# Kernel optimization log

Hardware: AMD Instinct MI355X
Metric: run time of the kernel (lower is better)

## Reference

```python
import jax, jax.numpy as jnp
import numpy as np
from jax import lax

T = 36          # sequence length
N_POLES = 80    # N -> dictionary has 2N+1 = 161 atoms
LAM = 0.1       # lam_f
MAX_ITER = 100
TOL = 1e-05


def real_D(T, rho, theta):
    # CONSTR=True: squash rho into [0.001, 1.15], theta into [0, pi]
    rmin, rmax = 0.001, 1.15
    r = rmin + (rmax - rmin) * jax.nn.sigmoid(rho)          # (N,)
    th = jnp.pi * jax.nn.sigmoid(theta)                     # (N,)
    i = jnp.arange(T, dtype=rho.dtype)[:, None]             # (T,1)
    p = r[None, :] ** i                                     # (T,N)
    W1 = p * jnp.cos(i * th[None, :])
    W2 = p * jnp.sin(i * th[None, :])
    D = jnp.concatenate([jnp.ones((T, 1), rho.dtype), W1, W2], axis=1)  # (T, 2N+1)
    # NORM=True: column-normalize all but the constant column
    norms = jnp.linalg.norm(D[:, 1:], axis=0, keepdims=True)
    return jnp.concatenate([D[:, :1], D[:, 1:] / norms], axis=1)


def softshrink(v, thr):
    return jnp.sign(v) * jnp.maximum(jnp.abs(v) - thr, 0.0)


def fista_efc(D, Y, lam, max_iter):
    # argmin_C ||Y - D C||_2^2 + lam |C|_1
    DtD = D.T @ D                                           # (P,P)
    L_inv = 1.0 / jnp.linalg.norm(DtD, ord=2)               # 1/spectral norm
    P = DtD.shape[0]
    dim_data = Y.shape[-1]
    A = jnp.eye(P, dtype=Y.dtype) - L_inv * DtD             # (P,P)
    B = L_inv * jnp.einsum('tp,btd->bpd', D, Y)             # (B,P,d)
    thr = lax.stop_gradient(lam * L_inv)                    # .item() in torch => constant

    batch = Y.shape[0]
    x0 = jnp.zeros((batch, P, dim_data), Y.dtype)
    y0 = jnp.zeros((batch, P, dim_data), Y.dtype)

    def body(carry, _):
        x, y, t, done = carry
        x_new = softshrink(jnp.einsum('pq,bqd->bpd', A, y) + B, thr)
        diff = jnp.linalg.norm(x - x_new) / dim_data        # Frobenius over all elems
        t_new = (1.0 + jnp.sqrt(1.0 + 4.0 * t * t)) / 2.0
        tt = (t - 1.0) / t_new
        y_new = (1.0 + tt) * x_new - tt * x
        # if already converged before this step, freeze the state (early return)
        x_out = jnp.where(done, x, x_new)
        y_out = jnp.where(done, y, y_new)
        t_out = jnp.where(done, t, t_new)
        done_new = done | (diff < TOL)
        return (x_out, y_out, t_out, done_new), None

    init = (x0, y0, jnp.float32(1.0), jnp.bool_(False))
    (x_fin, _, _, _), _ = lax.scan(body, init, None, length=max_iter)
    return x_fin


def reference(x, rho, theta):
    # DAN.forward with wiRH=False, freezeD=False
    dic = real_D(T, rho, theta)                             # (T, 2N+1)
    C = fista_efc(dic, x, LAM, MAX_ITER)                    # (B, 2N+1, d)
    reconst = jnp.einsum('tp,bpd->btd', dic, C)             # (B, T, d)
    return C, dic, reconst


def setup_inputs() -> dict:
    key = jax.random.key(0)
    k1, k2, k3 = jax.random.split(key, 3)
    x = jax.random.normal(k1, (256, T, 50), dtype=jnp.float32)
    rho = jax.random.uniform(k2, (N_POLES,), dtype=jnp.float32)
    theta = jax.random.uniform(k3, (N_POLES,), dtype=jnp.float32)
    return {"x": x, "rho": rho, "theta": theta}
```

## Files before the change

### kernel.cpp

```cpp
#include <hip/hip_runtime.h>
#include <math.h>

typedef _Float16 half_t;
typedef __attribute__((ext_vector_type(8))) _Float16 half8;
typedef __attribute__((ext_vector_type(4))) _Float16 half4;
typedef __attribute__((ext_vector_type(4))) float floatx4;

#define TDIM 36
#define PDIM 161
#define NCOL 50
#define NITER 100
#define PITER8 50

#define NKA 5
#define GSTR 44
#define SPS 196

#define YROW 384
#define RROW 128

#define SWZ(row, byteoff) ((byteoff) ^ (((row) & 7) << 4))

#define BY_Y    0
#define BY_R    24576
#define BY_LRTH 28672
#define BY_Y0   32768
#define BY_SC   33024
#define BY_GS   33040
#define BY_G2   39376
#define BY_G4   45712
#define LDS_TOTAL 52048

#define MFMA16 __builtin_amdgcn_mfma_f32_16x16x32_f16

__global__ __launch_bounds__(768, 3)
void dan_kernel(const float* __restrict__ xin, const float* __restrict__ rho,
                const float* __restrict__ theta, float* __restrict__ outC,
                float* __restrict__ outDic, float* __restrict__ outR)
{
  extern __shared__ char smc[];
  float*  sc   = (float*)(smc + BY_SC);
  float*  Gs   = (float*)(smc + BY_GS);
  float*  G2   = (float*)(smc + BY_G2);
  float*  G4   = (float*)(smc + BY_G4);
  float*  Y0f  = (float*)(smc + BY_Y0);
  float*  Df   = (float*)(smc + BY_Y);
  float*  lrth = (float*)(smc + BY_LRTH);

  const int tid = threadIdx.x;
  const int b = blockIdx.x;
  const int wave = tid >> 6, lane = tid & 63;
  const int q = lane >> 4, ln = lane & 15;

  {
    unsigned int* z = (unsigned int*)smc;
    for (int i = tid; i < LDS_TOTAL / 4; i += 768) z[i] = 0u;
  }
  __syncthreads();

  if (tid >= 1 && tid < PDIM) {
    const bool is_sin = tid > 80;
    const int n = is_sin ? (tid - 81) : (tid - 1);
    lrth[tid]       = logf(0.001f + 1.149f / (1.0f + expf(-rho[n])));
    lrth[161 + tid] = 3.14159265358979f / (1.0f + expf(-theta[n]));
  }
  __syncthreads();

  for (int i = tid; i < TDIM * PDIM; i += 768) {
    const int t = i / PDIM, p = i - t * PDIM;
    float val;
    if (p == 0) {
      val = 1.0f;
    } else {
      const float ft = (float)t;
      const float e = expf(ft * lrth[p]);
      const float ang = ft * lrth[161 + p];
      val = e * (p > 80 ? sinf(ang) : cosf(ang));
    }
    Df[t * SPS + p] = val;
  }
  __syncthreads();

  if (tid >= 1 && tid < PDIM) {
    float s2 = 0.0f;
    for (int t = 0; t < TDIM; ++t) {
      const float v = Df[t * SPS + tid];
      s2 += v * v;
    }
    const float inv = 1.0f / sqrtf(s2);
    for (int t = 0; t < TDIM; ++t) Df[t * SPS + tid] *= inv;
  }
  __syncthreads();

  if (tid < 666) {
    int i = 0, rem = tid;
    while (rem >= TDIM - i) { rem -= TDIM - i; ++i; }
    const int j = i + rem;
    const float4* ri = (const float4*)(Df + i * SPS);
    const float4* rj = (const float4*)(Df + j * SPS);
    float a = 0.0f;
    #pragma unroll 7
    for (int k = 0; k < SPS / 4; ++k) {
      const float4 x = ri[k], y = rj[k];
      a += x.x * y.x + x.y * y.y + x.z * y.z + x.w * y.w;
    }
    Gs[i * GSTR + j] = a;
    Gs[j * GSTR + i] = a;
  }
  if (b == 0) {
    for (int i = tid; i < TDIM * PDIM; i += 768) {
      const int t = i / PDIM, p = i - t * PDIM;
      outDic[i] = Df[t * SPS + p];
    }
  }

  const int mtA = wave >> 2;
  const int ntA = wave & 3;
  const int g = wave >> 1;
  const int h = wave & 1;

  half8 DhF[NKA], DlF[NKA];
  {
    const int row = 16 * mtA + ln;
    #pragma unroll
    for (int ks = 0; ks < NKA; ++ks) {
      half8 hh, ll;
      #pragma unroll
      for (int e = 0; e < 8; ++e) {
        const int p = 32 * ks + 8 * q + e + 1;
        const float v = (row < TDIM) ? Df[row * SPS + p] : 0.0f;
        const half_t h2 = (half_t)v;
        hh[e] = h2;
        ll[e] = (half_t)(v - (float)h2);
      }
      DhF[ks] = hh;
      DlF[ks] = ll;
    }
  }
  half8 DtH[2][2], DtL[2][2];
  #pragma unroll
  for (int k = 0; k < 2; ++k) {
    const int pt = g + 6 * k;
    if (pt < 10) {
      const int atom = 16 * pt + ln + 1;
      #pragma unroll
      for (int ks = 0; ks < 2; ++ks) {
        half8 hh, ll;
        #pragma unroll
        for (int e = 0; e < 8; ++e) {
          const int t = 32 * ks + 8 * q + e;
          const float v = (t < TDIM) ? Df[t * SPS + atom] : 0.0f;
          const half_t h2 = (half_t)v;
          hh[e] = h2;
          ll[e] = (half_t)(v - (float)h2);
        }
        DtH[k][ks] = hh;
        DtL[k][ks] = ll;
      }
    }
  }
  float yA[4];
  {
    const float* xb = xin + b * TDIM * NCOL;
    const int c = 16 * ntA + ln;
    #pragma unroll
    for (int r = 0; r < 4; ++r) {
      const int t = 16 * mtA + 4 * q + r;
      yA[r] = (t < TDIM && c < NCOL) ? xb[t * NCOL + c] : 0.0f;
    }
  }
  __syncthreads();

  if (tid < 666) {
    int i = 0, rem = tid;
    while (rem >= TDIM - i) { rem -= TDIM - i; ++i; }
    const int j = i + rem;
    const float4* ri = (const float4*)(Gs + i * GSTR);
    const float4* rj = (const float4*)(Gs + j * GSTR);
    float a = 0.0f;
    #pragma unroll
    for (int k = 0; k < GSTR / 4; ++k) {
      const float4 x = ri[k], y = rj[k];
      a += x.x * y.x + x.y * y.y + x.z * y.z + x.w * y.w;
    }
    G2[i * GSTR + j] = a;
    G2[j * GSTR + i] = a;
  }
  __syncthreads();
  if (tid < 666) {
    int i = 0, rem = tid;
    while (rem >= TDIM - i) { rem -= TDIM - i; ++i; }
    const int j = i + rem;
    const float4* ri = (const float4*)(G2 + i * GSTR);
    const float4* rj = (const float4*)(G2 + j * GSTR);
    float a = 0.0f;
    #pragma unroll
    for (int k = 0; k < GSTR / 4; ++k) {
      const float4 x = ri[k], y = rj[k];
      a += x.x * y.x + x.y * y.y + x.z * y.z + x.w * y.w;
    }
    G4[i * GSTR + j] = a;
    G4[j * GSTR + i] = a;
  }
  __syncthreads();
  if (tid < 666) {
    int i = 0, rem = tid;
    while (rem >= TDIM - i) { rem -= TDIM - i; ++i; }
    const int j = i + rem;
    const float4* ri = (const float4*)(G4 + i * GSTR);
    const float4* rj = (const float4*)(G4 + j * GSTR);
    float a = 0.0f;
    #pragma unroll
    for (int k = 0; k < GSTR / 4; ++k) {
      const float4 x = ri[k], y = rj[k];
      a += x.x * y.x + x.y * y.y + x.z * y.z + x.w * y.w;
    }
    G2[i * GSTR + j] = a;
    G2[j * GSTR + i] = a;
  }
  __syncthreads();

  if (wave == 0) {
    float g8r[36];
    #pragma unroll
    for (int j = 0; j < 36; ++j) g8r[j] = (lane < 36) ? G2[lane * GSTR + j] : 0.0f;
    float v = (lane < 36) ? 1.0f : 0.0f;
    for (int it = 0; it < PITER8; ++it) {
      const int vi = __float_as_int(v);
      float w0 = 0.0f, w1 = 0.0f, w2 = 0.0f, w3 = 0.0f;
      #pragma unroll
      for (int j = 0; j < 36; j += 4) {
        w0 = fmaf(g8r[j],     __int_as_float(__builtin_amdgcn_readlane(vi, j)),     w0);
        w1 = fmaf(g8r[j + 1], __int_as_float(__builtin_amdgcn_readlane(vi, j + 1)), w1);
        w2 = fmaf(g8r[j + 2], __int_as_float(__builtin_amdgcn_readlane(vi, j + 2)), w2);
        w3 = fmaf(g8r[j + 3], __int_as_float(__builtin_amdgcn_readlane(vi, j + 3)), w3);
      }
      float w = (w0 + w1) + (w2 + w3);
      float s = w * w;
      #pragma unroll
      for (int off = 32; off > 0; off >>= 1) s += __shfl_xor(s, off, 64);
      v = w * rsqrtf(s);
    }
    const int vi = __float_as_int(v);
    float w0 = 0.0f, w1 = 0.0f;
    #pragma unroll
    for (int j = 0; j < 36; j += 2) {
      const float gi0 = (lane < 36) ? Gs[lane * GSTR + j]     : 0.0f;
      const float gi1 = (lane < 36) ? Gs[lane * GSTR + j + 1] : 0.0f;
      w0 = fmaf(gi0, __int_as_float(__builtin_amdgcn_readlane(vi, j)),     w0);
      w1 = fmaf(gi1, __int_as_float(__builtin_amdgcn_readlane(vi, j + 1)), w1);
    }
    float num = v * (w0 + w1);
    #pragma unroll
    for (int off = 32; off > 0; off >>= 1) num += __shfl_xor(num, off, 64);
    if (lane == 0) {
      sc[0] = 1.0f / num;
      sc[1] = 0.1f / num;
    }
  } else {
    unsigned int* z = (unsigned int*)smc;
    for (int i = tid - 64; i < BY_SC / 4; i += 704) z[i] = 0u;
  }
  __syncthreads();
  const float L_inv = sc[0];
  const float thr = sc[1];

  float xR[2][2][4], yR[2][2][4];
  #pragma unroll
  for (int k = 0; k < 2; ++k)
    #pragma unroll
    for (int s = 0; s < 2; ++s)
      #pragma unroll
      for (int r = 0; r < 4; ++r) { xR[k][s][r] = 0.0f; yR[k][s][r] = 0.0f; }
  float x0v = 0.0f, y0v = 0.0f;

  float tk = 1.0f;

  for (int it = 0; it < NITER; ++it) {
    {
      const int n0 = 16 * ntA + ln;
      const float y0c = Y0f[n0];
      floatx4 aH0 = {0.f,0.f,0.f,0.f}, aH1 = {0.f,0.f,0.f,0.f};
      floatx4 aL0 = {0.f,0.f,0.f,0.f}, aL1 = {0.f,0.f,0.f,0.f};
      const char* yrow = smc + BY_Y + n0 * YROW;
      #pragma unroll
      for (int ks = 0; ks < NKA; ++ks) {
        const int kb = (32 * ks + 8 * q) * 2;
        const half8 b0 = *(const half8*)(yrow + SWZ(n0, kb));
        if (ks & 1) {
          aH1 = MFMA16(DhF[ks], b0, aH1, 0, 0, 0);
          aL1 = MFMA16(DlF[ks], b0, aL1, 0, 0, 0);
        } else {
          aH0 = MFMA16(DhF[ks], b0, aH0, 0, 0, 0);
          aL0 = MFMA16(DlF[ks], b0, aL0, 0, 0, 0);
        }
      }
      const int t0 = 16 * mtA + 4 * q;
      const bool tval = (t0 < TDIM);
      half4 hv;
      #pragma unroll
      for (int r = 0; r < 4; ++r)
        hv[r] = tval ? (half_t)(yA[r] - y0c - ((aH0[r] + aH1[r]) + (aL0[r] + aL1[r])))
                     : (half_t)0.0f;
      *(half4*)(smc + BY_R + n0 * RROW + SWZ(n0, t0 * 2)) = hv;
    }
    __syncthreads();

    const float tnew = 0.5f * (1.0f + sqrtf(1.0f + 4.0f * tk * tk));
    const float ttf = (tk - 1.0f) / tnew;
    tk = tnew;

    {
      half8 rb[2][2];
      #pragma unroll
      for (int s = 0; s < 2; ++s) {
        const int cS = 16 * (2 * h + s) + ln;
        const char* rrow = smc + BY_R + cS * RROW;
        rb[s][0] = *(const half8*)(rrow + SWZ(cS, 16 * q));
        rb[s][1] = *(const half8*)(rrow + SWZ(cS, 64 + 16 * q));
      }

      if (g == 5) {
        float p0 = 0.0f, p1 = 0.0f;
        #pragma unroll
        for (int e = 0; e < 8; ++e) {
          p0 += (float)rb[0][0][e] + (float)rb[0][1][e];
          p1 += (float)rb[1][0][e] + (float)rb[1][1][e];
        }
        p0 += __shfl_xor(p0, 16, 64);  p0 += __shfl_xor(p0, 32, 64);
        p1 += __shfl_xor(p1, 16, 64);  p1 += __shfl_xor(p1, 32, 64);
        if (q < 2) {
          const float part = (q & 1) ? p1 : p0;
          const int cSel = 16 * (2 * h + (q & 1)) + ln;
          const float w = y0v + L_inv * part;
          const float cl = fminf(fmaxf(w, -thr), thr);
          const float xn = w - cl;
          const float yn = xn + ttf * (xn - x0v);
          x0v = xn;
          y0v = yn;
          Y0f[cSel] = yn;
        }
      }

      #pragma unroll
      for (int k = 0; k < 2; ++k) {
        const int pt = g + 6 * k;
        if (pt < 10) {
          #pragma unroll
          for (int s = 0; s < 2; ++s) {
            floatx4 a = {0.f,0.f,0.f,0.f};
            a = MFMA16(DtH[k][0], rb[s][0], a, 0, 0, 0);
            a = MFMA16(DtL[k][0], rb[s][0], a, 0, 0, 0);
            a = MFMA16(DtH[k][1], rb[s][1], a, 0, 0, 0);
            a = MFMA16(DtL[k][1], rb[s][1], a, 0, 0, 0);
            const int cS = 16 * (2 * h + s) + ln;
            const int s0_ = 16 * pt + 4 * q;
            half4 hv;
            #pragma unroll
            for (int r = 0; r < 4; ++r) {
              const float w = yR[k][s][r] + L_inv * a[r];
              const float cl = fminf(fmaxf(w, -thr), thr);
              const float xn = w - cl;
              const float yn = xn + ttf * (xn - xR[k][s][r]);
              xR[k][s][r] = xn;
              yR[k][s][r] = yn;
              hv[r] = (half_t)yn;
            }
            *(half4*)(smc + BY_Y + cS * YROW + SWZ(cS, s0_ * 2)) = hv;
          }
        }
      }
    }
    __syncthreads();
  }

  float* Cb = outC + b * PDIM * NCOL;
  #pragma unroll
  for (int k = 0; k < 2; ++k) {
    const int pt = g + 6 * k;
    if (pt < 10) {
      #pragma unroll
      for (int s = 0; s < 2; ++s) {
        const int cS = 16 * (2 * h + s) + ln;
        if (cS < NCOL) {
          #pragma unroll
          for (int r = 0; r < 4; ++r)
            Cb[(16 * pt + 4 * q + r + 1) * NCOL + cS] = xR[k][s][r];
        }
      }
    }
  }
  if (g == 5 && q < 2) {
    const int cSel = 16 * (2 * h + (q & 1)) + ln;
    if (cSel < NCOL) Cb[cSel] = x0v;
  }
  #pragma unroll
  for (int k = 0; k < 2; ++k) {
    const int pt = g + 6 * k;
    if (pt < 10) {
      #pragma unroll
      for (int s = 0; s < 2; ++s) {
        const int cS = 16 * (2 * h + s) + ln;
        const int s0_ = 16 * pt + 4 * q;
        half4 hv;
        #pragma unroll
        for (int r = 0; r < 4; ++r) hv[r] = (half_t)xR[k][s][r];
        *(half4*)(smc + BY_Y + cS * YROW + SWZ(cS, s0_ * 2)) = hv;
      }
    }
  }
  if (g == 5 && q < 2) {
    const int cSel = 16 * (2 * h + (q & 1)) + ln;
    Y0f[cSel] = x0v;
  }
  __syncthreads();
  {
    const int n0 = 16 * ntA + ln;
    const float x0c = Y0f[n0];
    floatx4 aH0 = {0.f,0.f,0.f,0.f}, aH1 = {0.f,0.f,0.f,0.f};
    floatx4 aL0 = {0.f,0.f,0.f,0.f}, aL1 = {0.f,0.f,0.f,0.f};
    const char* yrow = smc + BY_Y + n0 * YROW;
    #pragma unroll
    for (int ks = 0; ks < NKA; ++ks) {
      const int kb = (32 * ks + 8 * q) * 2;
      const half8 b0 = *(const half8*)(yrow + SWZ(n0, kb));
      if (ks & 1) {
        aH1 = MFMA16(DhF[ks], b0, aH1, 0, 0, 0);
        aL1 = MFMA16(DlF[ks], b0, aL1, 0, 0, 0);
      } else {
        aH0 = MFMA16(DhF[ks], b0, aH0, 0, 0, 0);
        aL0 = MFMA16(DlF[ks], b0, aL0, 0, 0, 0);
      }
    }
    float* Rb = outR + b * TDIM * NCOL;
    const int c = n0;
    if (c < NCOL) {
      const int t0 = 16 * mtA + 4 * q;
      #pragma unroll
      for (int r = 0; r < 4; ++r) {
        const int t = t0 + r;
        if (t < TDIM)
          Rb[t * NCOL + c] = x0c + (aH0[r] + aH1[r]) + (aL0[r] + aL1[r]);
      }
    }
  }
}


extern "C" void kernel_launch(void* const* d_in, const int* in_sizes, int n_in,
                              void* d_out, int out_size, void* d_ws, size_t ws_size,
                              hipStream_t stream) {
  const float* x     = (const float*)d_in[0];
  const float* rho   = (const float*)d_in[1];
  const float* theta = (const float*)d_in[2];

  float* out    = (float*)d_out;
  float* outC   = out;
  float* outDic = out + 256 * PDIM * NCOL;
  float* outR   = outDic + TDIM * PDIM;

  hipLaunchKernelGGL(dan_kernel, dim3(256), dim3(768), LDS_TOTAL, stream,
                     x, rho, theta, outC, outDic, outR);
}
```

Baseline: 245.9 us.

## Fold constant atom into MFMA tiles and drop low-half split in D^T product

Moves the constant dictionary column into the regular MFMA tiling by widening the K loop to six slices and covering all 11 atom tiles per wave. This removes the special-case scalar reduction wave, its shuffles and the Y0 shared buffer. It also drops the fp16 low-part correction MFMAs in the D^T·R step, halving that product's MFMA count. In exchange it adds one extra MFMA pair per iteration in the forward product and lowers precision in the gradient step, which could change convergence accuracy.

```diff
diff --git a/kernel.cpp b/kernel.cpp
--- a/kernel.cpp
+++ b/kernel.cpp
@@ -12,7 +12,7 @@
 #define NITER 100
 #define PITER8 50
 
-#define NKA 5
+#define NKA 6
 #define GSTR 44
 #define SPS 196
 
@@ -24,12 +24,11 @@
 #define BY_Y    0
 #define BY_R    24576
 #define BY_LRTH 28672
-#define BY_Y0   32768
-#define BY_SC   33024
-#define BY_GS   33040
-#define BY_G2   39376
-#define BY_G4   45712
-#define LDS_TOTAL 52048
+#define BY_SC   32768
+#define BY_GS   32784
+#define BY_G2   39120
+#define BY_G4   45456
+#define LDS_TOTAL 51792
 
 #define MFMA16 __builtin_amdgcn_mfma_f32_16x16x32_f16
 
@@ -43,7 +42,6 @@
   float*  Gs   = (float*)(smc + BY_GS);
   float*  G2   = (float*)(smc + BY_G2);
   float*  G4   = (float*)(smc + BY_G4);
-  float*  Y0f  = (float*)(smc + BY_Y0);
   float*  Df   = (float*)(smc + BY_Y);
   float*  lrth = (float*)(smc + BY_LRTH);
 
@@ -124,39 +122,36 @@
     const int row = 16 * mtA + ln;
     #pragma unroll
     for (int ks = 0; ks < NKA; ++ks) {
-      half8 hh, ll;
-      #pragma unroll
-      for (int e = 0; e < 8; ++e) {
-        const int p = 32 * ks + 8 * q + e + 1;
-        const float v = (row < TDIM) ? Df[row * SPS + p] : 0.0f;
-        const half_t h2 = (half_t)v;
-        hh[e] = h2;
-        ll[e] = (half_t)(v - (float)h2);
+      half8 hh = {0,0,0,0,0,0,0,0}, ll = {0,0,0,0,0,0,0,0};
+      if (row < TDIM) {
+        const float4 f0 = *(const float4*)(Df + row * SPS + 32 * ks + 8 * q);
+        const float4 f1 = *(const float4*)(Df + row * SPS + 32 * ks + 8 * q + 4);
+        const float fa[8] = {f0.x, f0.y, f0.z, f0.w, f1.x, f1.y, f1.z, f1.w};
+        #pragma unroll
+        for (int e = 0; e < 8; ++e) {
+          const half_t h2 = (half_t)fa[e];
+          hh[e] = h2;
+          ll[e] = (half_t)(fa[e] - (float)h2);
+        }
       }
       DhF[ks] = hh;
       DlF[ks] = ll;
     }
   }
-  half8 DtH[2][2], DtL[2][2];
+  half8 DtH[2][2];
   #pragma unroll
   for (int k = 0; k < 2; ++k) {
-    const int pt = g + 6 * k;
-    if (pt < 10) {
-      const int atom = 16 * pt + ln + 1;
-      #pragma unroll
-      for (int ks = 0; ks < 2; ++ks) {
-        half8 hh, ll;
-        #pragma unroll
-        for (int e = 0; e < 8; ++e) {
-          const int t = 32 * ks + 8 * q + e;
-          const float v = (t < TDIM) ? Df[t * SPS + atom] : 0.0f;
-          const half_t h2 = (half_t)v;
-          hh[e] = h2;
-          ll[e] = (half_t)(v - (float)h2);
-        }
-        DtH[k][ks] = hh;
-        DtL[k][ks] = ll;
-      }
+    const int atom = 16 * (g + 6 * k) + ln;
+    #pragma unroll
+    for (int ks = 0; ks < 2; ++ks) {
+      half8 hh;
+      #pragma unroll
+      for (int e = 0; e < 8; ++e) {
+        const int t = 32 * ks + 8 * q + e;
+        const float v = (t < TDIM) ? Df[t * SPS + atom] : 0.0f;
+        hh[e] = (half_t)v;
+      }
+      DtH[k][ks] = hh;
     }
   }
   float yA[4];
@@ -259,7 +254,7 @@
     }
   } else {
     unsigned int* z = (unsigned int*)smc;
-    for (int i = tid - 64; i < BY_SC / 4; i += 704) z[i] = 0u;
+    for (int i = tid - 64; i < 32768 / 4; i += 704) z[i] = 0u;
   }
   __syncthreads();
   const float L_inv = sc[0];
@@ -272,16 +267,14 @@
     for (int s = 0; s < 2; ++s)
       #pragma unroll
       for (int r = 0; r < 4; ++r) { xR[k][s][r] = 0.0f; yR[k][s][r] = 0.0f; }
-  float x0v = 0.0f, y0v = 0.0f;
 
   float tk = 1.0f;
 
   for (int it = 0; it < NITER; ++it) {
     {
-      const int n0 = 16 * ntA + ln;
-      const float y0c = Y0f[n0];
       floatx4 aH0 = {0.f,0.f,0.f,0.f}, aH1 = {0.f,0.f,0.f,0.f};
       floatx4 aL0 = {0.f,0.f,0.f,0.f}, aL1 = {0.f,0.f,0.f,0.f};
+      const int n0 = 16 * ntA + ln;
       const char* yrow = smc + BY_Y + n0 * YROW;
       #pragma unroll
       for (int ks = 0; ks < NKA; ++ks) {
@@ -296,12 +289,10 @@
         }
       }
       const int t0 = 16 * mtA + 4 * q;
-      const bool tval = (t0 < TDIM);
       half4 hv;
       #pragma unroll
       for (int r = 0; r < 4; ++r)
-        hv[r] = tval ? (half_t)(yA[r] - y0c - ((aH0[r] + aH1[r]) + (aL0[r] + aL1[r])))
-                     : (half_t)0.0f;
+        hv[r] = (half_t)(yA[r] - ((aH0[r] + aH1[r]) + (aL0[r] + aL1[r])));
       *(half4*)(smc + BY_R + n0 * RROW + SWZ(n0, t0 * 2)) = hv;
     }
     __syncthreads();
@@ -320,54 +311,28 @@
         rb[s][1] = *(const half8*)(rrow + SWZ(cS, 64 + 16 * q));
       }
 
-      if (g == 5) {
-        float p0 = 0.0f, p1 = 0.0f;
-        #pragma unroll
-        for (int e = 0; e < 8; ++e) {
-          p0 += (float)rb[0][0][e] + (float)rb[0][1][e];
-          p1 += (float)rb[1][0][e] + (float)rb[1][1][e];
-        }
-        p0 += __shfl_xor(p0, 16, 64);  p0 += __shfl_xor(p0, 32, 64);
-        p1 += __shfl_xor(p1, 16, 64);  p1 += __shfl_xor(p1, 32, 64);
-        if (q < 2) {
-          const float part = (q & 1) ? p1 : p0;
-          const int cSel = 16 * (2 * h + (q & 1)) + ln;
-          const float w = y0v + L_inv * part;
-          const float cl = fminf(fmaxf(w, -thr), thr);
-          const float xn = w - cl;
-          const float yn = xn + ttf * (xn - x0v);
-          x0v = xn;
-          y0v = yn;
-          Y0f[cSel] = yn;
-        }
-      }
-
       #pragma unroll
       for (int k = 0; k < 2; ++k) {
         const int pt = g + 6 * k;
-        if (pt < 10) {
+        const int p0 = 16 * pt + 4 * q;
+        #pragma unroll
+        for (int s = 0; s < 2; ++s) {
+          floatx4 a = {0.f,0.f,0.f,0.f};
+          a = MFMA16(DtH[k][0], rb[s][0], a, 0, 0, 0);
+          a = MFMA16(DtH[k][1], rb[s][1], a, 0, 0, 0);
+          const int cS = 16 * (2 * h + s) + ln;
+          half4 hv;
           #pragma unroll
-          for (int s = 0; s < 2; ++s) {
-            floatx4 a = {0.f,0.f,0.f,0.f};
-            a = MFMA16(DtH[k][0], rb[s][0], a, 0, 0, 0);
-            a = MFMA16(DtL[k][0], rb[s][0], a, 0, 0, 0);
-            a = MFMA16(DtH[k][1], rb[s][1], a, 0, 0, 0);
-            a = MFMA16(DtL[k][1], rb[s][1], a, 0, 0, 0);
-            const int cS = 16 * (2 * h + s) + ln;
-            const int s0_ = 16 * pt + 4 * q;
-            half4 hv;
-            #pragma unroll
-            for (int r = 0; r < 4; ++r) {
-              const float w = yR[k][s][r] + L_inv * a[r];
-              const float cl = fminf(fmaxf(w, -thr), thr);
-              const float xn = w - cl;
-              const float yn = xn + ttf * (xn - xR[k][s][r]);
-              xR[k][s][r] = xn;
-              yR[k][s][r] = yn;
-              hv[r] = (half_t)yn;
-            }
-            *(half4*)(smc + BY_Y + cS * YROW + SWZ(cS, s0_ * 2)) = hv;
+          for (int r = 0; r < 4; ++r) {
+            const float w = yR[k][s][r] + L_inv * a[r];
+            const float cl = fminf(fmaxf(w, -thr), thr);
+            const float xn = w - cl;
+            const float yn = xn + ttf * (xn - xR[k][s][r]);
+            xR[k][s][r] = xn;
+            yR[k][s][r] = yn;
+            hv[r] = (half_t)yn;
           }
+          *(half4*)(smc + BY_Y + cS * YROW + SWZ(cS, p0 * 2)) = hv;
         }
       }
     }
@@ -378,47 +343,36 @@
   #pragma unroll
   for (int k = 0; k < 2; ++k) {
     const int pt = g + 6 * k;
-    if (pt < 10) {
-      #pragma unroll
-      for (int s = 0; s < 2; ++s) {
-        const int cS = 16 * (2 * h + s) + ln;
-        if (cS < NCOL) {
-          #pragma unroll
-          for (int r = 0; r < 4; ++r)
-            Cb[(16 * pt + 4 * q + r + 1) * NCOL + cS] = xR[k][s][r];
+    #pragma unroll
+    for (int s = 0; s < 2; ++s) {
+      const int cS = 16 * (2 * h + s) + ln;
+      if (cS < NCOL) {
+        #pragma unroll
+        for (int r = 0; r < 4; ++r) {
+          const int p = 16 * pt + 4 * q + r;
+          if (p < PDIM) Cb[p * NCOL + cS] = xR[k][s][r];
         }
       }
     }
-  }
-  if (g == 5 && q < 2) {
-    const int cSel = 16 * (2 * h + (q & 1)) + ln;
-    if (cSel < NCOL) Cb[cSel] = x0v;
   }
   #pragma unroll
   for (int k = 0; k < 2; ++k) {
     const int pt = g + 6 * k;
-    if (pt < 10) {
-      #pragma unroll
-      for (int s = 0; s < 2; ++s) {
-        const int cS = 16 * (2 * h + s) + ln;
-        const int s0_ = 16 * pt + 4 * q;
-        half4 hv;
-        #pragma unroll
-        for (int r = 0; r < 4; ++r) hv[r] = (half_t)xR[k][s][r];
-        *(half4*)(smc + BY_Y + cS * YROW + SWZ(cS, s0_ * 2)) = hv;
-      }
-    }
-  }
-  if (g == 5 && q < 2) {
-    const int cSel = 16 * (2 * h + (q & 1)) + ln;
-    Y0f[cSel] = x0v;
+    const int p0 = 16 * pt + 4 * q;
+    #pragma unroll
+    for (int s = 0; s < 2; ++s) {
+      const int cS = 16 * (2 * h + s) + ln;
+      half4 hv;
+      #pragma unroll
+      for (int r = 0; r < 4; ++r) hv[r] = (half_t)xR[k][s][r];
+      *(half4*)(smc + BY_Y + cS * YROW + SWZ(cS, p0 * 2)) = hv;
+    }
   }
   __syncthreads();
   {
-    const int n0 = 16 * ntA + ln;
-    const float x0c = Y0f[n0];
     floatx4 aH0 = {0.f,0.f,0.f,0.f}, aH1 = {0.f,0.f,0.f,0.f};
     floatx4 aL0 = {0.f,0.f,0.f,0.f}, aL1 = {0.f,0.f,0.f,0.f};
+    const int n0 = 16 * ntA + ln;
     const char* yrow = smc + BY_Y + n0 * YROW;
     #pragma unroll
     for (int ks = 0; ks < NKA; ++ks) {
@@ -440,7 +394,7 @@
       for (int r = 0; r < 4; ++r) {
         const int t = t0 + r;
         if (t < TDIM)
-          Rb[t * NCOL + c] = x0c + (aH0[r] + aH1[r]) + (aL0[r] + aL1[r]);
+          Rb[t * NCOL + c] = (aH0[r] + aH1[r]) + (aL0[r] + aL1[r]);
       }
     }
   }
```

Result: faster. 210.9 us (-14.2%).
